# Performance work log

Hardware: AMD Instinct MI355X
Metric: run time of the kernel (lower is better)

Reference implementation:

```python
import jax, jax.numpy as jnp
import numpy as np

R = 4096          # proposals per image
D = 4096          # fc7 feature dim (VGG16)
C = 20            # foreground classes (VOC); logits have C+1 with background
IMG_W, IMG_H = 1216.0, 800.0
SCORE_THRESH = 0.05
NMS_THRESH = 0.5
TOPK = 100


def setup_inputs() -> dict:
    key = jax.random.key(0)
    k1, k2, k3, k4, k5 = jax.random.split(key, 5)
    x = jax.random.normal(k1, (R, D), dtype=jnp.float32)
    # build valid xyxy boxes inside the image
    xy = jax.random.uniform(k2, (R, 2)) * jnp.array([IMG_W * 0.8, IMG_H * 0.8])
    wh = jax.random.uniform(k3, (R, 2)) * jnp.array([IMG_W * 0.4, IMG_H * 0.4]) + 8.0
    boxes = jnp.concatenate([xy, xy + wh], axis=1).astype(jnp.float32)
    W_cls = (jax.random.normal(k4, (D, C + 1)) * 0.01).astype(jnp.float32)
    W_det = (jax.random.normal(k5, (D, C + 1)) * 0.01).astype(jnp.float32)
    b_cls = jnp.zeros((C + 1,), jnp.float32)
    b_det = jnp.zeros((C + 1,), jnp.float32)
    return {"x": x, "boxes": boxes, "W_cls": W_cls, "b_cls": b_cls,
            "W_det": W_det, "b_det": b_det}


def _iou_matrix(b):
    # b: (R, 4) xyxy -> (R, R) IoU
    area = (b[:, 2] - b[:, 0]) * (b[:, 3] - b[:, 1])
    lt = jnp.maximum(b[:, None, :2], b[None, :, :2])
    rb = jnp.minimum(b[:, None, 2:], b[None, :, 2:])
    wh = jnp.clip(rb - lt, 0.0)
    inter = wh[..., 0] * wh[..., 1]
    return inter / (area[:, None] + area[None, :] - inter + 1e-9)


def _nms_per_class(sc, iou):
    # sc: (R,) scores for one class; iou: (R, R) shared IoU matrix.
    # Sequential greedy NMS over score-descending order; returns bool keep mask.
    n = sc.shape[0]
    order = jnp.argsort(-sc)

    def step(supp, oi):
        kept = (sc[oi] > SCORE_THRESH) & jnp.logical_not(supp[oi])
        supp = jnp.where(kept, supp | (iou[oi] > NMS_THRESH), supp)
        return supp, kept

    _, keep_sorted = jax.lax.scan(step, jnp.zeros((n,), bool), order)
    return jnp.zeros((n,), bool).at[order].set(keep_sorted)


def reference(x, boxes, W_cls, b_cls, W_det, b_det):
    # WSDDN two-stream head: class softmax x proposal softmax
    cls_logits = x @ W_cls + b_cls                      # (R, C+1)
    det_logits = x @ W_det + b_det                      # (R, C+1)
    scores = jax.nn.softmax(cls_logits, axis=1) * jax.nn.softmax(det_logits, axis=0)
    scores = scores[:, :-1]                             # drop background column (R, C)

    # clip boxes to image (Boxes.clip)
    b = jnp.stack([jnp.clip(boxes[:, 0], 0.0, IMG_W),
                   jnp.clip(boxes[:, 1], 0.0, IMG_H),
                   jnp.clip(boxes[:, 2], 0.0, IMG_W),
                   jnp.clip(boxes[:, 3], 0.0, IMG_H)], axis=1)

    iou = _iou_matrix(b)                                # (R, R)
    # per-class NMS (batched_nms with class-agnostic boxes == independent per-class NMS)
    keep = jax.vmap(lambda s: _nms_per_class(s, iou), in_axes=1, out_axes=1)(scores)  # (R, C)

    kept_scores = scores * keep.astype(scores.dtype)
    flat = kept_scores.reshape(-1)                      # (R*C,)
    top_vals, top_idx = jax.lax.top_k(flat, TOPK)
    top_prop = top_idx // C
    top_cls = top_idx % C
    top_boxes = b[top_prop]                             # (TOPK, 4)
    return top_vals, top_boxes, top_cls
```

## Files before the change

kernel.cpp:

```cpp
#include <hip/hip_runtime.h>
#include <math.h>

#define R_N 4096
#define D_N 4096
#define C_N 20
#define IMG_W_F 1216.0f
#define IMG_H_F 800.0f
#define SCORE_TH 0.05f
#define NMS_TH 0.5f
#define TOPK_N 100

#define WF_WORDS   (128 * 2 * 64 * 4)
#define DET_OFF    (WF_WORDS)
#define DET_WORDS  (R_N * 24)
#define CTRL_OFF   (DET_OFF + DET_WORDS)
#define CAND_R_OFF (CTRL_OFF + 64)
#define CAND_D_OFF (CAND_R_OFF + 640)
#define CAND_S_OFF (CAND_D_OFF + 640)

typedef short bf16x8 __attribute__((ext_vector_type(8)));
typedef float f32x4  __attribute__((ext_vector_type(4)));

__device__ __forceinline__ unsigned pk(float a, float b) {
  return __builtin_amdgcn_perm(__float_as_uint(a), __float_as_uint(b), 0x07060302u);
}
__device__ __forceinline__ float fexp(float x) { return __expf(x); }

__global__ __launch_bounds__(256) void wT_kernel(
    const float* __restrict__ Wd, uint4* __restrict__ Wfrag,
    float* __restrict__ ctrl) {
  const int e = blockIdx.x * 256 + threadIdx.x;
  const int l = e & 63;
  const int ct = (e >> 6) & 1;
  const int gs = e >> 7;
  const int c = ct * 16 + (l & 15);
  const int k0 = gs * 32 + (l >> 4) * 8;
  float w[8];
  if (c < 21) {
#pragma unroll
    for (int j = 0; j < 8; j++) w[j] = Wd[(size_t)(k0 + j) * 21 + c];
  } else {
#pragma unroll
    for (int j = 0; j < 8; j++) w[j] = 0.f;
  }
  uint4 v;
  v.x = pk(w[1], w[0]); v.y = pk(w[3], w[2]);
  v.z = pk(w[5], w[4]); v.w = pk(w[7], w[6]);
  Wfrag[(gs * 2 + ct) * 64 + l] = v;
  if (e < 64) ctrl[e] = 0.f;
}

__global__ __launch_bounds__(1024) void detgemm_kernel(
    const float* __restrict__ x, const uint4* __restrict__ Wfrag,
    float* __restrict__ detlog, float* __restrict__ dsum) {
  __shared__ float red[16 * 512];
  const int t = threadIdx.x;
  const int w = t >> 6, l = t & 63;
  const int r16 = l & 15, q = l >> 4;
  const int r0 = blockIdx.x * 16;

  const float* xrow = x + (size_t)(r0 + r16) * D_N + w * 256 + q * 8;
  f32x4 acc0 = {0.f, 0.f, 0.f, 0.f};
  f32x4 acc1 = {0.f, 0.f, 0.f, 0.f};

#pragma unroll
  for (int s = 0; s < 8; s++) {
    float4 a0 = *(const float4*)(xrow + s * 32);
    float4 a1 = *(const float4*)(xrow + s * 32 + 4);
    const int gs = w * 8 + s;
    union { uint4 u; bf16x8 v; } b0, b1;
    b0.u = Wfrag[(gs * 2 + 0) * 64 + l];
    b1.u = Wfrag[(gs * 2 + 1) * 64 + l];
    union { bf16x8 v; unsigned u[4]; } af;
    af.u[0] = pk(a0.y, a0.x);
    af.u[1] = pk(a0.w, a0.z);
    af.u[2] = pk(a1.y, a1.x);
    af.u[3] = pk(a1.w, a1.z);
    acc0 = __builtin_amdgcn_mfma_f32_16x16x32_bf16(af.v, b0.v, acc0, 0, 0, 0);
    acc1 = __builtin_amdgcn_mfma_f32_16x16x32_bf16(af.v, b1.v, acc1, 0, 0, 0);
  }

  *(f32x4*)(&red[w * 512 + (0  + r16) * 16 + q * 4]) = acc0;
  *(f32x4*)(&red[w * 512 + (16 + r16) * 16 + q * 4]) = acc1;
  __syncthreads();
  if (t < 512) {
    float v = 0.f;
#pragma unroll
    for (int w2 = 0; w2 < 16; w2++) v += red[w2 * 512 + t];
    red[t] = v;
  }
  __syncthreads();
  if (t < 21) {
    float s = 0.f;
#pragma unroll
    for (int r = 0; r < 16; r++) {
      float v = red[t * 16 + r];
      detlog[(size_t)(r0 + r) * 24 + t] = v;
      s += fexp(v);
    }
    atomicAdd(&dsum[t], s);
  }
}

__device__ __forceinline__ void load_clip_box(const float* boxes, int r, float* b) {
  b[0] = fminf(fmaxf(boxes[r * 4 + 0], 0.f), IMG_W_F);
  b[1] = fminf(fmaxf(boxes[r * 4 + 1], 0.f), IMG_H_F);
  b[2] = fminf(fmaxf(boxes[r * 4 + 2], 0.f), IMG_W_F);
  b[3] = fminf(fmaxf(boxes[r * 4 + 3], 0.f), IMG_H_F);
}

__global__ __launch_bounds__(256) void finish_kernel(
    const float* __restrict__ x, const float* __restrict__ Wc,
    const float* __restrict__ b_cls, const float* __restrict__ detlog,
    const float* __restrict__ dsum, int* __restrict__ nc, int* __restrict__ done,
    int* __restrict__ cand_r, float* __restrict__ cand_d, float* __restrict__ cand_s,
    const float* __restrict__ boxes, float* __restrict__ out) {
  __shared__ float sd[20];
  __shared__ bool s_last;
  const int t = threadIdx.x;
  if (t < 20) sd[t] = dsum[t];
  __syncthreads();

  const int r = blockIdx.x * 256 + t;
  for (int c = 0; c < 20; c++) {
    float dsm = fexp(detlog[(size_t)r * 24 + c]) / sd[c];
    if (dsm > SCORE_TH) {
      int p = atomicAdd(&nc[c], 1);
      if (p < 32) { cand_r[c * 32 + p] = r; cand_d[c * 32 + p] = dsm; }
    }
  }
  __threadfence();
  __syncthreads();
  if (t == 0) s_last = (atomicAdd(done, 1) == 15);
  __syncthreads();
  if (!s_last) return;
  __threadfence();

  for (int slot = t; slot < 640; slot += 256) {
    const int c = slot >> 5, i = slot & 31;
    int n = nc[c]; if (n > 32) n = 32;
    if (i < n) {
      const int rr = cand_r[slot];
      float lg[21];
#pragma unroll
      for (int j = 0; j < 21; j++) lg[j] = b_cls[j];
      const float* xr = x + (size_t)rr * D_N;
      for (int k = 0; k < D_N; k++) {
        float xv = xr[k];
        const float* wr = Wc + (size_t)k * 21;
#pragma unroll
        for (int j = 0; j < 21; j++) lg[j] = fmaf(xv, wr[j], lg[j]);
      }
      float m = -1e30f;
#pragma unroll
      for (int j = 0; j < 21; j++) m = fmaxf(m, lg[j]);
      float s = 0.f;
#pragma unroll
      for (int j = 0; j < 21; j++) s += fexp(lg[j] - m);
      float p = fexp(lg[c] - m) / s;
      cand_s[slot] = p * cand_d[slot];
    }
  }
  __syncthreads();

  __shared__ int   s_kc;
  __shared__ int   s_ki[512];
  __shared__ float s_ks[512];
  __shared__ float sval[TOPK_N];
  __shared__ int   sidx[TOPK_N];
  if (t == 0) s_kc = 0;
  if (t < TOPK_N) { sval[t] = 0.f; sidx[t] = 0; }
  __syncthreads();

  if (t < 20) {
    const int c = t;
    int n = nc[c]; if (n > 32) n = 32;
    float s[32]; int rr[32]; int n2 = 0;
    for (int i = 0; i < n; i++) {
      float sc = cand_s[c * 32 + i];
      if (sc > SCORE_TH) { s[n2] = sc; rr[n2] = cand_r[c * 32 + i]; n2++; }
    }
    for (int i = 1; i < n2; i++) {
      float si = s[i]; int ri = rr[i];
      int j = i - 1;
      while (j >= 0 && (s[j] < si || (s[j] == si && rr[j] > ri))) {
        s[j + 1] = s[j]; rr[j + 1] = rr[j]; j--;
      }
      s[j + 1] = si; rr[j + 1] = ri;
    }
    unsigned supp = 0;
    for (int i = 0; i < n2; i++) {
      if (supp & (1u << i)) continue;
      int g = atomicAdd(&s_kc, 1);
      if (g < 512) { s_ki[g] = rr[i] * C_N + c; s_ks[g] = s[i]; }
      float bi[4]; load_clip_box(boxes, rr[i], bi);
      float ai = (bi[2] - bi[0]) * (bi[3] - bi[1]);
      for (int j = i + 1; j < n2; j++) {
        if (supp & (1u << j)) continue;
        float bj[4]; load_clip_box(boxes, rr[j], bj);
        float aj = (bj[2] - bj[0]) * (bj[3] - bj[1]);
        float lx = fmaxf(bi[0], bj[0]), ly = fmaxf(bi[1], bj[1]);
        float rx = fminf(bi[2], bj[2]), ry = fminf(bi[3], bj[3]);
        float wdt = fmaxf(rx - lx, 0.f), hgt = fmaxf(ry - ly, 0.f);
        float inter = wdt * hgt;
        float iou = inter / (ai + aj - inter + 1e-9f);
        if (iou > NMS_TH) supp |= (1u << j);
      }
    }
  }
  __syncthreads();

  int m = s_kc; if (m > 512) m = 512;
  for (int i = t; i < m; i += 256) {
    float si = s_ks[i]; int xi = s_ki[i];
    int rank = 0;
    for (int j = 0; j < m; j++) {
      float sj = s_ks[j]; int xj = s_ki[j];
      if (sj > si || (sj == si && xj < xi)) rank++;
    }
    if (rank < TOPK_N) { sval[rank] = si; sidx[rank] = xi; }
  }
  __syncthreads();
  if (t == 0) {
    int f = m < TOPK_N ? m : TOPK_N;
    int cur = 0;
    for (int slot = f; slot < TOPK_N; slot++) {
      for (;;) {
        bool member = false;
        for (int j = 0; j < m; j++)
          if (s_ki[j] == cur) { member = true; break; }
        if (!member) break;
        cur++;
      }
      sval[slot] = 0.f;
      sidx[slot] = cur;
      cur++;
    }
  }
  __syncthreads();
  if (t < TOPK_N) {
    int idx = sidx[t];
    int prop = idx / C_N;
    int cls = idx - prop * C_N;
    float b[4]; load_clip_box(boxes, prop, b);
    out[t] = sval[t];
    out[TOPK_N + t * 4 + 0] = b[0];
    out[TOPK_N + t * 4 + 1] = b[1];
    out[TOPK_N + t * 4 + 2] = b[2];
    out[TOPK_N + t * 4 + 3] = b[3];
    out[TOPK_N * 5 + t] = (float)cls;
  }
}

extern "C" void kernel_launch(void* const* d_in, const int* in_sizes, int n_in,
                              void* d_out, int out_size, void* d_ws, size_t ws_size,
                              hipStream_t stream) {
  const float* x     = (const float*)d_in[0];
  const float* boxes = (const float*)d_in[1];
  const float* W_cls = (const float*)d_in[2];
  const float* b_cls = (const float*)d_in[3];
  const float* W_det = (const float*)d_in[4];

  float* out = (float*)d_out;
  float* ws = (float*)d_ws;
  uint4* Wfrag    = (uint4*)ws;
  float* detlog   = ws + DET_OFF;
  float* dsum     = ws + CTRL_OFF;
  int*   nc       = (int*)(ws + CTRL_OFF) + 24;
  int*   done     = (int*)(ws + CTRL_OFF) + 44;
  int*   cand_r   = (int*)(ws + CAND_R_OFF);
  float* cand_d   = ws + CAND_D_OFF;
  float* cand_s   = ws + CAND_S_OFF;

  wT_kernel     <<<64,  256,  0, stream>>>(W_det, Wfrag, dsum);
  detgemm_kernel<<<256, 1024, 0, stream>>>(x, Wfrag, detlog, dsum);
  finish_kernel <<<16,  256,  0, stream>>>(x, W_cls, b_cls, detlog, dsum,
                                           nc, done, cand_r, cand_d, cand_s,
                                           boxes, out);
}
```

Measured before the change: 124.0 us.

## Fuse finish stage into detection GEMM via last-block-done pattern

Drops the separate finish kernel. The last block of the detection GEMM, found with an atomic done counter, now runs candidate selection, the class-logit recompute, NMS and top-k. The GEMM also stores exp(logits) directly, so the finish stage no longer recomputes the exponential. This removes one kernel launch and the grid-wide handoff, but the candidate scan over 4096 proposals now runs in a single block where it used to be spread over 16 blocks.

```diff
diff --git a/kernel.cpp b/kernel.cpp
--- a/kernel.cpp
+++ b/kernel.cpp
@@ -11,9 +11,9 @@
 #define TOPK_N 100
 
 #define WF_WORDS   (128 * 2 * 64 * 4)
-#define DET_OFF    (WF_WORDS)
-#define DET_WORDS  (R_N * 24)
-#define CTRL_OFF   (DET_OFF + DET_WORDS)
+#define EDET_OFF   (WF_WORDS)
+#define EDET_WORDS (R_N * 24)
+#define CTRL_OFF   (EDET_OFF + EDET_WORDS)
 #define CAND_R_OFF (CTRL_OFF + 64)
 #define CAND_D_OFF (CAND_R_OFF + 640)
 #define CAND_S_OFF (CAND_D_OFF + 640)
@@ -25,6 +25,13 @@
   return __builtin_amdgcn_perm(__float_as_uint(a), __float_as_uint(b), 0x07060302u);
 }
 __device__ __forceinline__ float fexp(float x) { return __expf(x); }
+
+__device__ __forceinline__ void load_clip_box(const float* boxes, int r, float* b) {
+  b[0] = fminf(fmaxf(boxes[r * 4 + 0], 0.f), IMG_W_F);
+  b[1] = fminf(fmaxf(boxes[r * 4 + 1], 0.f), IMG_H_F);
+  b[2] = fminf(fmaxf(boxes[r * 4 + 2], 0.f), IMG_W_F);
+  b[3] = fminf(fmaxf(boxes[r * 4 + 3], 0.f), IMG_H_F);
+}
 
 __global__ __launch_bounds__(256) void wT_kernel(
     const float* __restrict__ Wd, uint4* __restrict__ Wfrag,
@@ -52,8 +59,15 @@
 
 __global__ __launch_bounds__(1024) void detgemm_kernel(
     const float* __restrict__ x, const uint4* __restrict__ Wfrag,
-    float* __restrict__ detlog, float* __restrict__ dsum) {
-  __shared__ float red[16 * 512];
+    const float* __restrict__ Wc, const float* __restrict__ b_cls,
+    const float* __restrict__ boxes,
+    float* __restrict__ edet, float* __restrict__ dsum,
+    int* __restrict__ nc, int* __restrict__ done,
+    int* __restrict__ cand_r, float* __restrict__ cand_d, float* __restrict__ cand_s,
+    float* __restrict__ out) {
+  __shared__ char smem[32768];
+  __shared__ bool s_last;
+  float* red = (float*)smem;
   const int t = threadIdx.x;
   const int w = t >> 6, l = t & 63;
   const int r16 = l & 15, q = l >> 4;
@@ -62,7 +76,6 @@
   const float* xrow = x + (size_t)(r0 + r16) * D_N + w * 256 + q * 8;
   f32x4 acc0 = {0.f, 0.f, 0.f, 0.f};
   f32x4 acc1 = {0.f, 0.f, 0.f, 0.f};
-
 #pragma unroll
   for (int s = 0; s < 8; s++) {
     float4 a0 = *(const float4*)(xrow + s * 32);
@@ -90,53 +103,48 @@
     red[t] = v;
   }
   __syncthreads();
-  if (t < 21) {
+  if (t < 20) {
     float s = 0.f;
 #pragma unroll
     for (int r = 0; r < 16; r++) {
-      float v = red[t * 16 + r];
-      detlog[(size_t)(r0 + r) * 24 + t] = v;
-      s += fexp(v);
+      float e = fexp(red[t * 16 + r]);
+      edet[(size_t)(r0 + r) * 24 + t] = e;
+      s += e;
     }
     atomicAdd(&dsum[t], s);
   }
-}
-
-__device__ __forceinline__ void load_clip_box(const float* boxes, int r, float* b) {
-  b[0] = fminf(fmaxf(boxes[r * 4 + 0], 0.f), IMG_W_F);
-  b[1] = fminf(fmaxf(boxes[r * 4 + 1], 0.f), IMG_H_F);
-  b[2] = fminf(fmaxf(boxes[r * 4 + 2], 0.f), IMG_W_F);
-  b[3] = fminf(fmaxf(boxes[r * 4 + 3], 0.f), IMG_H_F);
-}
-
-__global__ __launch_bounds__(256) void finish_kernel(
-    const float* __restrict__ x, const float* __restrict__ Wc,
-    const float* __restrict__ b_cls, const float* __restrict__ detlog,
-    const float* __restrict__ dsum, int* __restrict__ nc, int* __restrict__ done,
-    int* __restrict__ cand_r, float* __restrict__ cand_d, float* __restrict__ cand_s,
-    const float* __restrict__ boxes, float* __restrict__ out) {
-  __shared__ float sd[20];
-  __shared__ bool s_last;
-  const int t = threadIdx.x;
-  if (t < 20) sd[t] = dsum[t];
-  __syncthreads();
-
-  const int r = blockIdx.x * 256 + t;
-  for (int c = 0; c < 20; c++) {
-    float dsm = fexp(detlog[(size_t)r * 24 + c]) / sd[c];
-    if (dsm > SCORE_TH) {
-      int p = atomicAdd(&nc[c], 1);
-      if (p < 32) { cand_r[c * 32 + p] = r; cand_d[c * 32 + p] = dsm; }
-    }
-  }
   __threadfence();
   __syncthreads();
-  if (t == 0) s_last = (atomicAdd(done, 1) == 15);
+  if (t == 0) s_last = (atomicAdd(done, 1) == 255);
   __syncthreads();
   if (!s_last) return;
   __threadfence();
 
-  for (int slot = t; slot < 640; slot += 256) {
+  float* sd   = (float*)smem;
+  int*   s_kc = (int*)(smem + 128);
+  int*   s_ki = (int*)(smem + 256);
+  float* s_ks = (float*)(smem + 2304);
+  float* sval = (float*)(smem + 4352);
+  int*   sidx = (int*)(smem + 4864);
+  if (t < 20) sd[t] = dsum[t];
+  if (t == 0) *s_kc = 0;
+  if (t < TOPK_N) { sval[t] = 0.f; sidx[t] = 0; }
+  __syncthreads();
+
+#pragma unroll
+  for (int j = 0; j < 4; j++) {
+    const int r = t + j * 1024;
+    for (int c = 0; c < 20; c++) {
+      float dsm = edet[(size_t)r * 24 + c] / sd[c];
+      if (dsm > SCORE_TH) {
+        int p = atomicAdd(&nc[c], 1);
+        if (p < 32) { cand_r[c * 32 + p] = r; cand_d[c * 32 + p] = dsm; }
+      }
+    }
+  }
+  __syncthreads();
+
+  for (int slot = t; slot < 640; slot += 1024) {
     const int c = slot >> 5, i = slot & 31;
     int n = nc[c]; if (n > 32) n = 32;
     if (i < n) {
@@ -161,15 +169,6 @@
       cand_s[slot] = p * cand_d[slot];
     }
   }
-  __syncthreads();
-
-  __shared__ int   s_kc;
-  __shared__ int   s_ki[512];
-  __shared__ float s_ks[512];
-  __shared__ float sval[TOPK_N];
-  __shared__ int   sidx[TOPK_N];
-  if (t == 0) s_kc = 0;
-  if (t < TOPK_N) { sval[t] = 0.f; sidx[t] = 0; }
   __syncthreads();
 
   if (t < 20) {
@@ -191,7 +190,7 @@
     unsigned supp = 0;
     for (int i = 0; i < n2; i++) {
       if (supp & (1u << i)) continue;
-      int g = atomicAdd(&s_kc, 1);
+      int g = atomicAdd(s_kc, 1);
       if (g < 512) { s_ki[g] = rr[i] * C_N + c; s_ks[g] = s[i]; }
       float bi[4]; load_clip_box(boxes, rr[i], bi);
       float ai = (bi[2] - bi[0]) * (bi[3] - bi[1]);
@@ -210,8 +209,8 @@
   }
   __syncthreads();
 
-  int m = s_kc; if (m > 512) m = 512;
-  for (int i = t; i < m; i += 256) {
+  int m = *s_kc; if (m > 512) m = 512;
+  for (int i = t; i < m; i += 1024) {
     float si = s_ks[i]; int xi = s_ki[i];
     int rank = 0;
     for (int j = 0; j < m; j++) {
@@ -264,7 +263,7 @@
   float* out = (float*)d_out;
   float* ws = (float*)d_ws;
   uint4* Wfrag    = (uint4*)ws;
-  float* detlog   = ws + DET_OFF;
+  float* edet     = ws + EDET_OFF;
   float* dsum     = ws + CTRL_OFF;
   int*   nc       = (int*)(ws + CTRL_OFF) + 24;
   int*   done     = (int*)(ws + CTRL_OFF) + 44;
@@ -273,8 +272,7 @@
   float* cand_s   = ws + CAND_S_OFF;
 
   wT_kernel     <<<64,  256,  0, stream>>>(W_det, Wfrag, dsum);
-  detgemm_kernel<<<256, 1024, 0, stream>>>(x, Wfrag, detlog, dsum);
-  finish_kernel <<<16,  256,  0, stream>>>(x, W_cls, b_cls, detlog, dsum,
-                                           nc, done, cand_r, cand_d, cand_s,
-                                           boxes, out);
-}
+  detgemm_kernel<<<256, 1024, 0, stream>>>(x, Wfrag, W_cls, b_cls, boxes,
+                                           edet, dsum, nc, done,
+                                           cand_r, cand_d, cand_s, out);
+}
```

Result: slower. 235.4 us (+89.8%).
